# Kernel tuning notes

Hardware: AMD Instinct MI355X
Metric: run time of the kernel (lower is better)

The kernel has to match this reference:

```python
import jax, jax.numpy as jnp
import numpy as np

N = 50000   # nodes
E = 800000  # edges
F = 2       # num_feats
D = 2       # output_dim
H = 64      # hidden_size
L = 2       # num_layers
T = 12      # seq_len
HZN = 12    # horizon
NEG_SLOPE = 0.2


def setup_inputs() -> dict:
    key = jax.random.key(0)
    ks = jax.random.split(key, 10)
    x = jax.random.normal(ks[0], (T, N, F), dtype=jnp.float32)
    src = jax.random.randint(ks[1], (E,), 0, N, dtype=jnp.int32)
    dst = jax.random.randint(ks[2], (E,), 0, N, dtype=jnp.int32)

    def conv_params(k, fin):
        k1, k2, k3 = jax.random.split(k, 3)
        s = 1.0 / np.sqrt(fin)
        W = (jax.random.normal(k1, (3, fin, H), jnp.float32) * s)
        al = (jax.random.normal(k2, (3, H), jnp.float32) * s)
        ar = (jax.random.normal(k3, (3, H), jnp.float32) * s)
        b = jnp.zeros((3, H), jnp.float32)
        return W, al, ar, b

    enc_W0, enc_al0, enc_ar0, enc_b0 = conv_params(ks[3], F + H)
    enc_W1, enc_al1, enc_ar1, enc_b1 = conv_params(ks[4], 2 * H)
    dec_W0, dec_al0, dec_ar0, dec_b0 = conv_params(ks[5], D + H)
    dec_W1, dec_al1, dec_ar1, dec_b1 = conv_params(ks[6], 2 * H)
    proj_W = jax.random.normal(ks[7], (H, D), jnp.float32) / np.sqrt(H)
    proj_b = jnp.zeros((D,), jnp.float32)
    return dict(x=x, src=src, dst=dst,
                enc_W0=enc_W0, enc_al0=enc_al0, enc_ar0=enc_ar0, enc_b0=enc_b0,
                enc_W1=enc_W1, enc_al1=enc_al1, enc_ar1=enc_ar1, enc_b1=enc_b1,
                dec_W0=dec_W0, dec_al0=dec_al0, dec_ar0=dec_ar0, dec_b0=dec_b0,
                dec_W1=dec_W1, dec_al1=dec_al1, dec_ar1=dec_ar1, dec_b1=dec_b1,
                proj_W=proj_W, proj_b=proj_b)


def _gat(feat, W, al, ar, b, src, dst):
    # DGL GATConv, single head: fc -> edge attention -> edge softmax -> aggregate.
    h = feat @ W                              # [N, H]
    el = (h * al).sum(-1)                     # [N] source attention logits
    er = (h * ar).sum(-1)                     # [N] destination attention logits
    e = jax.nn.leaky_relu(el[src] + er[dst], NEG_SLOPE)   # [E]
    m = jax.ops.segment_max(e, dst, num_segments=N)       # per-dst max (stable softmax)
    ex = jnp.exp(e - m[dst])                               # [E]
    s = jax.ops.segment_sum(ex, dst, num_segments=N)       # [N]
    alpha = ex / jnp.maximum(s[dst], 1e-9)                 # [E] edge softmax
    out = jax.ops.segment_sum(h[src] * alpha[:, None], dst, num_segments=N)  # [N, H]
    return out + b


def _gru(xin, hx, W, al, ar, b, src, dst):
    iv = jnp.concatenate([xin, hx], axis=1)
    r = jax.nn.sigmoid(_gat(iv, W[0], al[0], ar[0], b[0], src, dst))
    z = jax.nn.sigmoid(_gat(iv, W[1], al[1], ar[1], b[1], src, dst))
    hc = jnp.tanh(_gat(jnp.concatenate([xin, r * hx], axis=1), W[2], al[2], ar[2], b[2], src, dst))
    return z * hx + (1.0 - z) * hc


def reference(x, src, dst,
              enc_W0, enc_al0, enc_ar0, enc_b0,
              enc_W1, enc_al1, enc_ar1, enc_b1,
              dec_W0, dec_al0, dec_ar0, dec_b0,
              dec_W1, dec_al1, dec_ar1, dec_b1,
              proj_W, proj_b):
    enc_params = [(enc_W0, enc_al0, enc_ar0, enc_b0), (enc_W1, enc_al1, enc_ar1, enc_b1)]
    dec_params = [(dec_W0, dec_al0, dec_ar0, dec_b0), (dec_W1, dec_al1, dec_ar1, dec_b1)]

    def enc_step(hstack, xt):
        out = xt
        new = []
        for i, (W, al, ar, b) in enumerate(enc_params):
            hn = _gru(out, hstack[i], W, al, ar, b, src, dst)
            new.append(hn)
            out = hn
        return jnp.stack(new), None

    h0 = jnp.zeros((L, N, H), x.dtype)
    hT, _ = jax.lax.scan(enc_step, h0, x)

    def dec_step(carry, _):
        dec_in, hstack = carry
        out = dec_in
        new = []
        for i, (W, al, ar, b) in enumerate(dec_params):
            hn = _gru(out, hstack[i], W, al, ar, b, src, dst)
            new.append(hn)
            out = hn
        pred = out @ proj_W + proj_b                 # [N, D]
        return (pred, jnp.stack(new)), pred

    dec_in0 = jnp.zeros((N, D), x.dtype)
    _, outputs = jax.lax.scan(dec_step, (dec_in0, hT), None, length=HZN)
    return outputs  # [horizon, N, output_dim]
```

## Files before the change

### kernel.cpp

```cpp
#include <hip/hip_runtime.h>
#include <hip/hip_bf16.h>

__device__ __forceinline__ float wsum64(float v) {
#pragma unroll
  for (int m = 32; m > 0; m >>= 1) v += __shfl_xor(v, m, 64);
  return v;
}
__device__ __forceinline__ float gsum16(float v) {
#pragma unroll
  for (int m = 8; m > 0; m >>= 1) v += __shfl_xor(v, m, 16);
  return v;
}
__device__ __forceinline__ float lrelu(float x) { return x > 0.f ? x : 0.2f * x; }
__device__ __forceinline__ float sigf(float x) { return 1.f / (1.f + __expf(-x)); }
__device__ __forceinline__ float dp4(float4 a, float4 b) {
  return a.x * b.x + a.y * b.y + a.z * b.z + a.w * b.w;
}

#define MM1P(P, f, row)                                    \
  {                                                        \
    float4 w_ = (P)[(row) * 16 + l16];                     \
    acc.x = fmaf((f), w_.x, acc.x);                        \
    acc.y = fmaf((f), w_.y, acc.y);                        \
    acc.z = fmaf((f), w_.z, acc.z);                        \
    acc.w = fmaf((f), w_.w, acc.w);                        \
  }

__global__ void hist_k(const int* __restrict__ dst, int* __restrict__ cnt, int e) {
  int i = blockIdx.x * blockDim.x + threadIdx.x;
  if (i < e) atomicAdd(&cnt[dst[i]], 1);
}

__global__ __launch_bounds__(256) void bsum_k(const int* __restrict__ cnt,
                                              int* __restrict__ bsum, int n) {
  __shared__ int red[4];
  int base = blockIdx.x * 1024;
  int t = threadIdx.x;
  int v = 0;
#pragma unroll
  for (int i = 0; i < 4; i++) {
    int idx = base + t + i * 256;
    v += (idx < n) ? cnt[idx] : 0;
  }
#pragma unroll
  for (int m = 32; m > 0; m >>= 1) v += __shfl_xor(v, m, 64);
  if ((t & 63) == 0) red[t >> 6] = v;
  __syncthreads();
  if (t == 0) bsum[blockIdx.x] = red[0] + red[1] + red[2] + red[3];
}

__global__ __launch_bounds__(1024) void scan_bsum_k(int* __restrict__ bsum,
                                                    int* __restrict__ rpn, int nb) {
  __shared__ int buf[1024];
  int t = threadIdx.x;
  int v = (t < nb) ? bsum[t] : 0;
  buf[t] = v;
  __syncthreads();
  int val = v;
  for (int off = 1; off < 1024; off <<= 1) {
    int u = (t >= off) ? buf[t - off] : 0;
    __syncthreads();
    val += u;
    buf[t] = val;
    __syncthreads();
  }
  if (t < nb) bsum[t] = val - v;
  if (t == nb - 1) *rpn = val;
}

__global__ __launch_bounds__(1024) void scan_fin_k(const int* __restrict__ cnt,
                                                   const int* __restrict__ bsum,
                                                   int* __restrict__ rp,
                                                   int* __restrict__ cursor, int n) {
  __shared__ int buf[1024];
  int t = threadIdx.x;
  int idx = blockIdx.x * 1024 + t;
  int v = (idx < n) ? cnt[idx] : 0;
  buf[t] = v;
  __syncthreads();
  int val = v;
  for (int off = 1; off < 1024; off <<= 1) {
    int u = (t >= off) ? buf[t - off] : 0;
    __syncthreads();
    val += u;
    buf[t] = val;
    __syncthreads();
  }
  if (idx < n) {
    int e = bsum[blockIdx.x] + val - v;
    rp[idx] = e;
    cursor[idx] = e;
  }
}

__global__ void scatter_k(const int* __restrict__ src, const int* __restrict__ dst,
                          int* __restrict__ cursor, int* __restrict__ srcs, int e) {
  int i = blockIdx.x * blockDim.x + threadIdx.x;
  if (i < e) {
    int pos = atomicAdd(&cursor[dst[i]], 1);
    srcs[pos] = src[i];
  }
}

template <int FA>
__global__ __launch_bounds__(512) void mm0_k(
    const float* __restrict__ xa, const float* __restrict__ xb,
    const float* __restrict__ Wg, const float* __restrict__ al, const float* __restrict__ ar,
    float* __restrict__ hb, float* __restrict__ el, float* __restrict__ er, int n) {
  constexpr int KP = FA + 64;
  __shared__ float Wl[KP * 128];
  __shared__ float Xl[32 * KP];
  for (int i = threadIdx.x; i < KP * 64; i += 512) {
    float2 wv = {Wg[i], Wg[(size_t)KP * 64 + i]};
    *(float2*)&Wl[i * 2] = wv;
  }
  int rbase = blockIdx.x * 32;
  for (int i = threadIdx.x; i < 32 * KP; i += 512) {
    int row = i / KP, k = i - row * KP;
    int r = rbase + row; if (r >= n) r = n - 1;
    Xl[i] = (k < FA) ? xa[(size_t)r * FA + k] : xb[(size_t)r * 64 + (k - FA)];
  }
  __syncthreads();
  int lane = threadIdx.x & 63, w = threadIdx.x >> 6;
  int rb = rbase + w * 4;
  if (rb >= n) return;
  float alr = al[lane], arr_ = ar[lane];
  float alz = al[64 + lane], arz = ar[64 + lane];
  float accr[4], accz[4];
#pragma unroll
  for (int i = 0; i < 4; i++) { accr[i] = 0.f; accz[i] = 0.f; }
  const int xoff = (w * 4) * KP;
#pragma unroll 8
  for (int k = 0; k < KP; k += 2) {
    float2 w0 = *(const float2*)&Wl[(k * 64 + lane) * 2];
    float2 w1 = *(const float2*)&Wl[((k + 1) * 64 + lane) * 2];
#pragma unroll
    for (int i = 0; i < 4; i++) {
      float2 xv = *(const float2*)&Xl[xoff + i * KP + k];
      accr[i] = fmaf(xv.x, w0.x, accr[i]);
      accz[i] = fmaf(xv.x, w0.y, accz[i]);
      accr[i] = fmaf(xv.y, w1.x, accr[i]);
      accz[i] = fmaf(xv.y, w1.y, accz[i]);
    }
  }
#pragma unroll
  for (int i = 0; i < 4; i++) {
    int r = rb + i;
    bool ok = r < n;
    if (ok) {
      hb[(size_t)r * 128 + lane] = accr[i];
      hb[(size_t)r * 128 + 64 + lane] = accz[i];
    }
    float s0 = wsum64(accr[i] * alr);
    float s1 = wsum64(accz[i] * alz);
    float s2 = wsum64(accr[i] * arr_);
    float s3 = wsum64(accz[i] * arz);
    if (ok && lane == 0) {
      el[(size_t)r * 2 + 0] = s0;
      el[(size_t)r * 2 + 1] = s1;
      er[(size_t)r * 2 + 0] = s2;
      er[(size_t)r * 2 + 1] = s3;
    }
  }
}

template <int FA>
__global__ __launch_bounds__(512) void kb_k(
    const int* __restrict__ rp, const int* __restrict__ srcs,
    const float* __restrict__ hbuf, const float* __restrict__ elrz,
    const float* __restrict__ errz, const float* __restrict__ b,
    const float* __restrict__ xa, const float* __restrict__ hx,
    const float* __restrict__ Wc, const float* __restrict__ alc,
    const float* __restrict__ arc,
    float* __restrict__ hc, float* __restrict__ elc, float* __restrict__ erc,
    float* __restrict__ zb, int n) {
  int l16 = threadIdx.x & 15;
  int d = blockIdx.x * 32 + (threadIdx.x >> 4);
  if (d >= n) return;
  int beg = rp[d], deg = rp[d + 1] - beg;
  float2 erd = ((const float2*)errz)[d];
  const float4* h4 = (const float4*)hbuf;
  float4 accr = {0, 0, 0, 0}, accz = {0, 0, 0, 0};
  float sr = 0.f, sz = 0.f;
  for (int base = 0; base < deg; base += 16) {
    int k = base + l16;
    int s = 0;
    float exr = 0.f, exz = 0.f;
    if (k < deg) {
      s = srcs[beg + k];
      float2 el = ((const float2*)elrz)[s];
      exr = __expf(lrelu(el.x + erd.x));
      exz = __expf(lrelu(el.y + erd.y));
      sr += exr; sz += exz;
    }
#pragma unroll
    for (int j = 0; j < 16; j++) {
      int sj = __shfl(s, j, 16);
      float aj = __shfl(exr, j, 16);
      float zj = __shfl(exz, j, 16);
      float4 hr = h4[(size_t)sj * 32 + l16];
      float4 hz = h4[(size_t)sj * 32 + 16 + l16];
      accr.x = fmaf(aj, hr.x, accr.x); accr.y = fmaf(aj, hr.y, accr.y);
      accr.z = fmaf(aj, hr.z, accr.z); accr.w = fmaf(aj, hr.w, accr.w);
      accz.x = fmaf(zj, hz.x, accz.x); accz.y = fmaf(zj, hz.y, accz.y);
      accz.z = fmaf(zj, hz.z, accz.z); accz.w = fmaf(zj, hz.w, accz.w);
    }
  }
  sr = gsum16(sr); sz = gsum16(sz);
  float invr = 1.f / fmaxf(sr, 1e-9f);
  float invz = 1.f / fmaxf(sz, 1e-9f);
  float4 br4 = ((const float4*)b)[l16];
  float4 bz4 = ((const float4*)(b + 64))[l16];
  float4 hx4 = ((const float4*)hx)[(size_t)d * 16 + l16];
  float4 rv, zv;
  rv.x = sigf(fmaf(accr.x, invr, br4.x)) * hx4.x;
  rv.y = sigf(fmaf(accr.y, invr, br4.y)) * hx4.y;
  rv.z = sigf(fmaf(accr.z, invr, br4.z)) * hx4.z;
  rv.w = sigf(fmaf(accr.w, invr, br4.w)) * hx4.w;
  zv.x = sigf(fmaf(accz.x, invz, bz4.x));
  zv.y = sigf(fmaf(accz.y, invz, bz4.y));
  zv.z = sigf(fmaf(accz.z, invz, bz4.z));
  zv.w = sigf(fmaf(accz.w, invz, bz4.w));
  ((float4*)zb)[(size_t)d * 16 + l16] = zv;
  const float4* Wr4 = (const float4*)(Wc + (size_t)FA * 64);
  const float4* Wx4 = (const float4*)Wc;
  float4 acc = {0, 0, 0, 0};
#pragma unroll 4
  for (int o = 0; o < 16; o++) {
    float f0 = __shfl(rv.x, o, 16);
    float f1 = __shfl(rv.y, o, 16);
    float f2 = __shfl(rv.z, o, 16);
    float f3 = __shfl(rv.w, o, 16);
    MM1P(Wr4, f0, 4 * o + 0); MM1P(Wr4, f1, 4 * o + 1);
    MM1P(Wr4, f2, 4 * o + 2); MM1P(Wr4, f3, 4 * o + 3);
  }
  if (FA == 2) {
    float f0 = xa[(size_t)d * 2 + 0];
    float f1 = xa[(size_t)d * 2 + 1];
    MM1P(Wx4, f0, 0); MM1P(Wx4, f1, 1);
  } else {
    float4 xv = ((const float4*)xa)[(size_t)d * 16 + l16];
#pragma unroll 4
    for (int o = 0; o < 16; o++) {
      float f0 = __shfl(xv.x, o, 16);
      float f1 = __shfl(xv.y, o, 16);
      float f2 = __shfl(xv.z, o, 16);
      float f3 = __shfl(xv.w, o, 16);
      MM1P(Wx4, f0, 4 * o + 0); MM1P(Wx4, f1, 4 * o + 1);
      MM1P(Wx4, f2, 4 * o + 2); MM1P(Wx4, f3, 4 * o + 3);
    }
  }
  float4 alv = ((const float4*)alc)[l16];
  float4 arv = ((const float4*)arc)[l16];
  float sl = gsum16(dp4(acc, alv));
  float sr2 = gsum16(dp4(acc, arv));
  if (l16 == 0) { elc[d] = sl; erc[d] = sr2; }
  ((float4*)hc)[(size_t)d * 16 + l16] = acc;
}

template <int FAN, bool NEXT>
__global__ __launch_bounds__(512) void kc_k(
    const int* __restrict__ rp, const int* __restrict__ srcs,
    const float* __restrict__ hc, const float* __restrict__ elc,
    const float* __restrict__ erc, const float* __restrict__ bc,
    const float* __restrict__ zb, float* __restrict__ hstate,
    const float* __restrict__ projW, const float* __restrict__ projb,
    float* __restrict__ outp,
    const float* __restrict__ Wn, const float* __restrict__ aln,
    const float* __restrict__ arn, const float* __restrict__ xan,
    const float* __restrict__ hxn,
    float* __restrict__ hbn, float* __restrict__ elrzn, float* __restrict__ errzn,
    int n) {
  constexpr int KPN = FAN + 64;
  int l16 = threadIdx.x & 15;
  int d = blockIdx.x * 32 + (threadIdx.x >> 4);
  if (d >= n) return;
  int beg = rp[d], deg = rp[d + 1] - beg;
  float erd = erc[d];
  const float4* h4 = (const float4*)hc;
  float4 acg = {0, 0, 0, 0};
  float ssum = 0.f;
  for (int base0 = 0; base0 < deg; base0 += 16) {
    int k = base0 + l16;
    int s = 0;
    float ex = 0.f;
    if (k < deg) {
      s = srcs[beg + k];
      ex = __expf(lrelu(elc[s] + erd));
      ssum += ex;
    }
#pragma unroll
    for (int j = 0; j < 16; j++) {
      int sj = __shfl(s, j, 16);
      float aj = __shfl(ex, j, 16);
      float4 hv = h4[(size_t)sj * 16 + l16];
      acg.x = fmaf(aj, hv.x, acg.x); acg.y = fmaf(aj, hv.y, acg.y);
      acg.z = fmaf(aj, hv.z, acg.z); acg.w = fmaf(aj, hv.w, acg.w);
    }
  }
  ssum = gsum16(ssum);
  float inv = 1.f / fmaxf(ssum, 1e-9f);
  float4 bc4 = ((const float4*)bc)[l16];
  float4 z4 = ((const float4*)zb)[(size_t)d * 16 + l16];
  float4 hx4 = ((const float4*)hstate)[(size_t)d * 16 + l16];
  float4 hcv, hn;
  hcv.x = tanhf(fmaf(acg.x, inv, bc4.x));
  hcv.y = tanhf(fmaf(acg.y, inv, bc4.y));
  hcv.z = tanhf(fmaf(acg.z, inv, bc4.z));
  hcv.w = tanhf(fmaf(acg.w, inv, bc4.w));
  hn.x = z4.x * hx4.x + (1.f - z4.x) * hcv.x;
  hn.y = z4.y * hx4.y + (1.f - z4.y) * hcv.y;
  hn.z = z4.z * hx4.z + (1.f - z4.z) * hcv.z;
  hn.w = z4.w * hx4.w + (1.f - z4.w) * hcv.w;
  ((float4*)hstate)[(size_t)d * 16 + l16] = hn;
  float p0 = 0.f, p1 = 0.f;
  if (outp) {
    const float4* wp4 = (const float4*)projW;
    float4 a0 = wp4[l16 * 2], a1 = wp4[l16 * 2 + 1];
    p0 = gsum16(hn.x * a0.x + hn.y * a0.z + hn.z * a1.x + hn.w * a1.z) + projb[0];
    p1 = gsum16(hn.x * a0.y + hn.y * a0.w + hn.z * a1.y + hn.w * a1.w) + projb[1];
    if (l16 == 0) {
      outp[(size_t)d * 2 + 0] = p0;
      outp[(size_t)d * 2 + 1] = p1;
    }
  }

  if constexpr (NEXT) {
    float4 hxn4 = ((const float4*)hxn)[(size_t)d * 16 + l16];
    float fa0 = 0.f, fa1 = 0.f;
    float4 xv = hn;
    if (FAN == 2) {
      if (xan) { fa0 = xan[(size_t)d * 2 + 0]; fa1 = xan[(size_t)d * 2 + 1]; }
      else { fa0 = p0; fa1 = p1; }
    }
#pragma unroll
    for (int g = 0; g < 2; g++) {
      const float4* Wh4 = (const float4*)(Wn + ((size_t)g * KPN + FAN) * 64);
      const float4* Wx4 = (const float4*)(Wn + (size_t)g * KPN * 64);
      float4 acc = {0, 0, 0, 0};
#pragma unroll 4
      for (int o = 0; o < 16; o++) {
        float f0 = __shfl(hxn4.x, o, 16);
        float f1 = __shfl(hxn4.y, o, 16);
        float f2 = __shfl(hxn4.z, o, 16);
        float f3 = __shfl(hxn4.w, o, 16);
        MM1P(Wh4, f0, 4 * o + 0); MM1P(Wh4, f1, 4 * o + 1);
        MM1P(Wh4, f2, 4 * o + 2); MM1P(Wh4, f3, 4 * o + 3);
      }
      if (FAN == 2) {
        MM1P(Wx4, fa0, 0); MM1P(Wx4, fa1, 1);
      } else {
#pragma unroll 4
        for (int o = 0; o < 16; o++) {
          float f0 = __shfl(xv.x, o, 16);
          float f1 = __shfl(xv.y, o, 16);
          float f2 = __shfl(xv.z, o, 16);
          float f3 = __shfl(xv.w, o, 16);
          MM1P(Wx4, f0, 4 * o + 0); MM1P(Wx4, f1, 4 * o + 1);
          MM1P(Wx4, f2, 4 * o + 2); MM1P(Wx4, f3, 4 * o + 3);
        }
      }
      float4 al4 = ((const float4*)aln)[g * 16 + l16];
      float4 ar4 = ((const float4*)arn)[g * 16 + l16];
      float eL = gsum16(dp4(acc, al4));
      float eR = gsum16(dp4(acc, ar4));
      if (l16 == 0) {
        elrzn[(size_t)d * 2 + g] = eL;
        errzn[(size_t)d * 2 + g] = eR;
      }
      ((float4*)hbn)[(size_t)d * 32 + g * 16 + l16] = acc;
    }
  }
}

extern "C" void kernel_launch(void* const* d_in, const int* in_sizes, int n_in,
                              void* d_out, int out_size, void* d_ws, size_t ws_size,
                              hipStream_t stream) {
  const int T = 12, F = 2, H = 64;
  const float* x = (const float*)d_in[0];
  const int* src = (const int*)d_in[1];
  const int* dst = (const int*)d_in[2];
  const float* Ws[4] = {(const float*)d_in[3], (const float*)d_in[7],
                        (const float*)d_in[11], (const float*)d_in[15]};
  const float* als[4] = {(const float*)d_in[4], (const float*)d_in[8],
                         (const float*)d_in[12], (const float*)d_in[16]};
  const float* ars[4] = {(const float*)d_in[5], (const float*)d_in[9],
                         (const float*)d_in[13], (const float*)d_in[17]};
  const float* bs[4] = {(const float*)d_in[6], (const float*)d_in[10],
                        (const float*)d_in[14], (const float*)d_in[18]};
  const float* proj_W = (const float*)d_in[19];
  const float* proj_b = (const float*)d_in[20];
  float* out = (float*)d_out;

  const int E = in_sizes[1];
  const int N = in_sizes[0] / (T * F);
  const int NB = (N + 1023) / 1024;

  char* wp = (char*)d_ws;
  size_t off = 0;
  auto carve = [&](size_t bytes) {
    void* p = wp + off;
    off = (off + bytes + 255) & ~(size_t)255;
    return p;
  };
  int* counts = (int*)carve((size_t)N * 4);
  int* bsum = (int*)carve((size_t)NB * 4);
  int* rp = (int*)carve((size_t)(N + 1) * 4);
  int* cursor = (int*)carve((size_t)N * 4);
  int* srcs = (int*)carve((size_t)E * 4);
  float* hs0 = (float*)carve((size_t)N * H * 4);
  float* hs1 = (float*)carve((size_t)N * H * 4);
  float* hbuf = (float*)carve((size_t)N * 2 * H * 4);
  float* elrz = (float*)carve((size_t)N * 2 * 4);
  float* errz = (float*)carve((size_t)N * 2 * 4);
  float* hcb = (float*)carve((size_t)N * H * 4);
  float* elc = (float*)carve((size_t)N * 4);
  float* erc = (float*)carve((size_t)N * 4);
  float* zbuf = (float*)carve((size_t)N * H * 4);
  float* zero2 = (float*)carve((size_t)N * F * 4);
  (void)ws_size;

  const int G_E = (E + 255) / 256;
  const int G32 = (N + 31) / 32;

  hipMemsetAsync(counts, 0, (size_t)N * 4, stream);
  hist_k<<<G_E, 256, 0, stream>>>(dst, counts, E);
  bsum_k<<<NB, 256, 0, stream>>>(counts, bsum, N);
  scan_bsum_k<<<1, 1024, 0, stream>>>(bsum, rp + N, NB);
  scan_fin_k<<<NB, 1024, 0, stream>>>(counts, bsum, rp, cursor, N);
  scatter_k<<<G_E, 256, 0, stream>>>(src, dst, cursor, srcs, E);

  hipMemsetAsync(hs0, 0, (size_t)N * H * 4, stream);
  hipMemsetAsync(hs1, 0, (size_t)N * H * 4, stream);
  hipMemsetAsync(zero2, 0, (size_t)N * F * 4, stream);

  mm0_k<2><<<G32, 512, 0, stream>>>(x, hs0, Ws[0], als[0], ars[0], hbuf, elrz, errz, N);

  for (int i = 0; i < 48; i++) {
    bool enc = i < 24;
    int j = enc ? i : i - 24;
    int t = j >> 1, layer = j & 1;
    int type = (enc ? 0 : 2) + layer;
    const float* W = Ws[type];
    const float* al = als[type];
    const float* ar = ars[type];
    const float* b = bs[type];
    int FA = layer ? 64 : 2;
    size_t KP = FA + 64;
    const float* Wc = W + (size_t)2 * KP * 64;
    const float* xa = layer ? hs0
                            : (enc ? x + (size_t)t * N * 2
                                   : (t == 0 ? zero2 : out + (size_t)(t - 1) * N * 2));
    float* hstate = layer ? hs1 : hs0;
    float* outp = (!enc && layer) ? out + (size_t)t * N * 2 : nullptr;

    if (FA == 2)
      kb_k<2><<<G32, 512, 0, stream>>>(rp, srcs, hbuf, elrz, errz, b, xa, hstate,
                                       Wc, al + 128, ar + 128, hcb, elc, erc, zbuf, N);
    else
      kb_k<64><<<G32, 512, 0, stream>>>(rp, srcs, hbuf, elrz, errz, b, xa, hstate,
                                        Wc, al + 128, ar + 128, hcb, elc, erc, zbuf, N);

    if (i == 47) {
      kc_k<2, false><<<G32, 512, 0, stream>>>(
          rp, srcs, hcb, elc, erc, b + 128, zbuf, hstate, proj_W, proj_b, outp,
          nullptr, nullptr, nullptr, nullptr, nullptr, nullptr, nullptr, nullptr, N);
    } else {
      int i2 = i + 1;
      bool enc2 = i2 < 24;
      int j2 = enc2 ? i2 : i2 - 24;
      int t2 = j2 >> 1, l2 = j2 & 1;
      int type2 = (enc2 ? 0 : 2) + l2;
      const float* Wn = Ws[type2];
      const float* aln = als[type2];
      const float* arn = ars[type2];
      const float* xan = nullptr;
      if (l2 == 0) {
        if (enc2) xan = x + (size_t)t2 * N * 2;
        else if (t2 == 0) xan = zero2;
      }
      const float* hxn = l2 ? hs1 : hs0;
      if (l2)
        kc_k<64, true><<<G32, 512, 0, stream>>>(
            rp, srcs, hcb, elc, erc, b + 128, zbuf, hstate, proj_W, proj_b, outp,
            Wn, aln, arn, xan, hxn, hbuf, elrz, errz, N);
      else
        kc_k<2, true><<<G32, 512, 0, stream>>>(
            rp, srcs, hcb, elc, erc, b + 128, zbuf, hstate, proj_W, proj_b, outp,
            Wn, aln, arn, xan, hxn, hbuf, elrz, errz, N);
    }
  }
  (void)out_size; (void)n_in;
}
```

Measured before the change: 9.444 ms.

## Unfuse next-step gate projection from kc_k and stage candidate weights in LDS

Removes the fused next-step r/z gate matmul from the kc_k epilogue and runs it again as a separate mm_k launch before each kb_k, using the LDS-tiled weight path. kb_k now copies the candidate weight matrix into shared memory (reordered hidden-first) and fully unrolls its per-node matmul loops, so weights are read from LDS instead of global/L2. This lowers register pressure and the redundant global weight reads in kc_k. In exchange it adds 48 extra kernel launches and an extra round trip through global memory for hbuf/elrz/errz.

```diff
diff --git a/kernel.cpp b/kernel.cpp
--- a/kernel.cpp
+++ b/kernel.cpp
@@ -17,9 +17,9 @@
   return a.x * b.x + a.y * b.y + a.z * b.z + a.w * b.w;
 }
 
-#define MM1P(P, f, row)                                    \
+#define MM1(f, row)                                        \
   {                                                        \
-    float4 w_ = (P)[(row) * 16 + l16];                     \
+    float4 w_ = W4[(row) * 16 + l16];                      \
     acc.x = fmaf((f), w_.x, acc.x);                        \
     acc.y = fmaf((f), w_.y, acc.y);                        \
     acc.z = fmaf((f), w_.z, acc.z);                        \
@@ -103,7 +103,7 @@
 }
 
 template <int FA>
-__global__ __launch_bounds__(512) void mm0_k(
+__global__ __launch_bounds__(512) void mm_k(
     const float* __restrict__ xa, const float* __restrict__ xb,
     const float* __restrict__ Wg, const float* __restrict__ al, const float* __restrict__ ar,
     float* __restrict__ hb, float* __restrict__ el, float* __restrict__ er, int n) {
@@ -174,6 +174,14 @@
     const float* __restrict__ arc,
     float* __restrict__ hc, float* __restrict__ elc, float* __restrict__ erc,
     float* __restrict__ zb, int n) {
+  constexpr int KP = FA + 64;
+  __shared__ float WlC[KP * 64];
+  for (int i = threadIdx.x; i < KP * 64; i += 512) {
+    int k = i >> 6, c = i & 63;
+    int ks = (k < 64) ? (FA + k) : (k - 64);
+    WlC[i] = Wc[(size_t)ks * 64 + c];
+  }
+  __syncthreads();
   int l16 = threadIdx.x & 15;
   int d = blockIdx.x * 32 + (threadIdx.x >> 4);
   if (d >= n) return;
@@ -222,32 +230,31 @@
   zv.z = sigf(fmaf(accz.z, invz, bz4.z));
   zv.w = sigf(fmaf(accz.w, invz, bz4.w));
   ((float4*)zb)[(size_t)d * 16 + l16] = zv;
-  const float4* Wr4 = (const float4*)(Wc + (size_t)FA * 64);
-  const float4* Wx4 = (const float4*)Wc;
+  const float4* W4 = (const float4*)WlC;
   float4 acc = {0, 0, 0, 0};
-#pragma unroll 4
+#pragma unroll
   for (int o = 0; o < 16; o++) {
     float f0 = __shfl(rv.x, o, 16);
     float f1 = __shfl(rv.y, o, 16);
     float f2 = __shfl(rv.z, o, 16);
     float f3 = __shfl(rv.w, o, 16);
-    MM1P(Wr4, f0, 4 * o + 0); MM1P(Wr4, f1, 4 * o + 1);
-    MM1P(Wr4, f2, 4 * o + 2); MM1P(Wr4, f3, 4 * o + 3);
+    MM1(f0, 4 * o + 0); MM1(f1, 4 * o + 1);
+    MM1(f2, 4 * o + 2); MM1(f3, 4 * o + 3);
   }
   if (FA == 2) {
     float f0 = xa[(size_t)d * 2 + 0];
     float f1 = xa[(size_t)d * 2 + 1];
-    MM1P(Wx4, f0, 0); MM1P(Wx4, f1, 1);
+    MM1(f0, 64); MM1(f1, 65);
   } else {
     float4 xv = ((const float4*)xa)[(size_t)d * 16 + l16];
-#pragma unroll 4
+#pragma unroll
     for (int o = 0; o < 16; o++) {
       float f0 = __shfl(xv.x, o, 16);
       float f1 = __shfl(xv.y, o, 16);
       float f2 = __shfl(xv.z, o, 16);
       float f3 = __shfl(xv.w, o, 16);
-      MM1P(Wx4, f0, 4 * o + 0); MM1P(Wx4, f1, 4 * o + 1);
-      MM1P(Wx4, f2, 4 * o + 2); MM1P(Wx4, f3, 4 * o + 3);
+      MM1(f0, 64 + 4 * o + 0); MM1(f1, 64 + 4 * o + 1);
+      MM1(f2, 64 + 4 * o + 2); MM1(f3, 64 + 4 * o + 3);
     }
   }
   float4 alv = ((const float4*)alc)[l16];
@@ -258,20 +265,13 @@
   ((float4*)hc)[(size_t)d * 16 + l16] = acc;
 }
 
-template <int FAN, bool NEXT>
 __global__ __launch_bounds__(512) void kc_k(
     const int* __restrict__ rp, const int* __restrict__ srcs,
     const float* __restrict__ hc, const float* __restrict__ elc,
     const float* __restrict__ erc, const float* __restrict__ bc,
     const float* __restrict__ zb, float* __restrict__ hstate,
     const float* __restrict__ projW, const float* __restrict__ projb,
-    float* __restrict__ outp,
-    const float* __restrict__ Wn, const float* __restrict__ aln,
-    const float* __restrict__ arn, const float* __restrict__ xan,
-    const float* __restrict__ hxn,
-    float* __restrict__ hbn, float* __restrict__ elrzn, float* __restrict__ errzn,
-    int n) {
-  constexpr int KPN = FAN + 64;
+    float* __restrict__ outp, int n) {
   int l16 = threadIdx.x & 15;
   int d = blockIdx.x * 32 + (threadIdx.x >> 4);
   if (d >= n) return;
@@ -313,62 +313,14 @@
   hn.z = z4.z * hx4.z + (1.f - z4.z) * hcv.z;
   hn.w = z4.w * hx4.w + (1.f - z4.w) * hcv.w;
   ((float4*)hstate)[(size_t)d * 16 + l16] = hn;
-  float p0 = 0.f, p1 = 0.f;
   if (outp) {
     const float4* wp4 = (const float4*)projW;
-    float4 a0 = wp4[l16 * 2], a1 = wp4[l16 * 2 + 1];
-    p0 = gsum16(hn.x * a0.x + hn.y * a0.z + hn.z * a1.x + hn.w * a1.z) + projb[0];
-    p1 = gsum16(hn.x * a0.y + hn.y * a0.w + hn.z * a1.y + hn.w * a1.w) + projb[1];
+    float4 a0p = wp4[l16 * 2], a1p = wp4[l16 * 2 + 1];
+    float p0 = gsum16(hn.x * a0p.x + hn.y * a0p.z + hn.z * a1p.x + hn.w * a1p.z) + projb[0];
+    float p1 = gsum16(hn.x * a0p.y + hn.y * a0p.w + hn.z * a1p.y + hn.w * a1p.w) + projb[1];
     if (l16 == 0) {
       outp[(size_t)d * 2 + 0] = p0;
       outp[(size_t)d * 2 + 1] = p1;
-    }
-  }
-
-  if constexpr (NEXT) {
-    float4 hxn4 = ((const float4*)hxn)[(size_t)d * 16 + l16];
-    float fa0 = 0.f, fa1 = 0.f;
-    float4 xv = hn;
-    if (FAN == 2) {
-      if (xan) { fa0 = xan[(size_t)d * 2 + 0]; fa1 = xan[(size_t)d * 2 + 1]; }
-      else { fa0 = p0; fa1 = p1; }
-    }
-#pragma unroll
-    for (int g = 0; g < 2; g++) {
-      const float4* Wh4 = (const float4*)(Wn + ((size_t)g * KPN + FAN) * 64);
-      const float4* Wx4 = (const float4*)(Wn + (size_t)g * KPN * 64);
-      float4 acc = {0, 0, 0, 0};
-#pragma unroll 4
-      for (int o = 0; o < 16; o++) {
-        float f0 = __shfl(hxn4.x, o, 16);
-        float f1 = __shfl(hxn4.y, o, 16);
-        float f2 = __shfl(hxn4.z, o, 16);
-        float f3 = __shfl(hxn4.w, o, 16);
-        MM1P(Wh4, f0, 4 * o + 0); MM1P(Wh4, f1, 4 * o + 1);
-        MM1P(Wh4, f2, 4 * o + 2); MM1P(Wh4, f3, 4 * o + 3);
-      }
-      if (FAN == 2) {
-        MM1P(Wx4, fa0, 0); MM1P(Wx4, fa1, 1);
-      } else {
-#pragma unroll 4
-        for (int o = 0; o < 16; o++) {
-          float f0 = __shfl(xv.x, o, 16);
-          float f1 = __shfl(xv.y, o, 16);
-          float f2 = __shfl(xv.z, o, 16);
-          float f3 = __shfl(xv.w, o, 16);
-          MM1P(Wx4, f0, 4 * o + 0); MM1P(Wx4, f1, 4 * o + 1);
-          MM1P(Wx4, f2, 4 * o + 2); MM1P(Wx4, f3, 4 * o + 3);
-        }
-      }
-      float4 al4 = ((const float4*)aln)[g * 16 + l16];
-      float4 ar4 = ((const float4*)arn)[g * 16 + l16];
-      float eL = gsum16(dp4(acc, al4));
-      float eR = gsum16(dp4(acc, ar4));
-      if (l16 == 0) {
-        elrzn[(size_t)d * 2 + g] = eL;
-        errzn[(size_t)d * 2 + g] = eR;
-      }
-      ((float4*)hbn)[(size_t)d * 32 + g * 16 + l16] = acc;
     }
   }
 }
@@ -434,8 +386,6 @@
   hipMemsetAsync(hs1, 0, (size_t)N * H * 4, stream);
   hipMemsetAsync(zero2, 0, (size_t)N * F * 4, stream);
 
-  mm0_k<2><<<G32, 512, 0, stream>>>(x, hs0, Ws[0], als[0], ars[0], hbuf, elrz, errz, N);
-
   for (int i = 0; i < 48; i++) {
     bool enc = i < 24;
     int j = enc ? i : i - 24;
@@ -454,41 +404,17 @@
     float* hstate = layer ? hs1 : hs0;
     float* outp = (!enc && layer) ? out + (size_t)t * N * 2 : nullptr;
 
-    if (FA == 2)
+    if (FA == 2) {
+      mm_k<2><<<G32, 512, 0, stream>>>(xa, hstate, W, al, ar, hbuf, elrz, errz, N);
       kb_k<2><<<G32, 512, 0, stream>>>(rp, srcs, hbuf, elrz, errz, b, xa, hstate,
                                        Wc, al + 128, ar + 128, hcb, elc, erc, zbuf, N);
-    else
+    } else {
+      mm_k<64><<<G32, 512, 0, stream>>>(xa, hstate, W, al, ar, hbuf, elrz, errz, N);
       kb_k<64><<<G32, 512, 0, stream>>>(rp, srcs, hbuf, elrz, errz, b, xa, hstate,
                                         Wc, al + 128, ar + 128, hcb, elc, erc, zbuf, N);
-
-    if (i == 47) {
-      kc_k<2, false><<<G32, 512, 0, stream>>>(
-          rp, srcs, hcb, elc, erc, b + 128, zbuf, hstate, proj_W, proj_b, outp,
-          nullptr, nullptr, nullptr, nullptr, nullptr, nullptr, nullptr, nullptr, N);
-    } else {
-      int i2 = i + 1;
-      bool enc2 = i2 < 24;
-      int j2 = enc2 ? i2 : i2 - 24;
-      int t2 = j2 >> 1, l2 = j2 & 1;
-      int type2 = (enc2 ? 0 : 2) + l2;
-      const float* Wn = Ws[type2];
-      const float* aln = als[type2];
-      const float* arn = ars[type2];
-      const float* xan = nullptr;
-      if (l2 == 0) {
-        if (enc2) xan = x + (size_t)t2 * N * 2;
-        else if (t2 == 0) xan = zero2;
-      }
-      const float* hxn = l2 ? hs1 : hs0;
-      if (l2)
-        kc_k<64, true><<<G32, 512, 0, stream>>>(
-            rp, srcs, hcb, elc, erc, b + 128, zbuf, hstate, proj_W, proj_b, outp,
-            Wn, aln, arn, xan, hxn, hbuf, elrz, errz, N);
-      else
-        kc_k<2, true><<<G32, 512, 0, stream>>>(
-            rp, srcs, hcb, elc, erc, b + 128, zbuf, hstate, proj_W, proj_b, outp,
-            Wn, aln, arn, xan, hxn, hbuf, elrz, errz, N);
-    }
+    }
+    kc_k<<<G32, 512, 0, stream>>>(rp, srcs, hcb, elc, erc, b + 128, zbuf, hstate,
+                                  proj_W, proj_b, outp, N);
   }
   (void)out_size; (void)n_in;
 }
```

Result: faster. 7.665 ms (-18.8%).
